# Optimization experiments

Hardware: AMD Instinct MI355X
Metric: run time of the kernel (lower is better)

The kernel has to match this reference:

```python
import jax, jax.numpy as jnp
import numpy as np
import math

N = 64
DIN = 2
DOUT = 2
D = 4
BATCH = 16384
EPS_DIV = 1e-6


def setup_inputs() -> dict:
    key = jax.random.key(0)
    k1, k2, k3 = jax.random.split(key, 3)
    x = jax.random.normal(k1, (BATCH, N, DIN), jnp.float32)
    # A scaled by 0.5 to keep 64-step products of DxD matrices inside float32 range
    A = jax.random.normal(k2, (N, D, D, DIN), jnp.float32) * 0.5
    B = jax.random.normal(k3, (N, D, D, DOUT, DIN), jnp.float32)
    scale = jnp.ones((1,), jnp.float32)
    return {"x": x, "A": A, "B": B, "scale": scale}


def _forward(x, A, B, scale):
    b, n, din = x.shape
    nbin = int(math.log(n - 1) / math.log(2.0)) + 1  # matches torch set_parallel_vars
    s = scale.reshape(())
    # per-site L2 normalization of input features (torch: X / ||X||, no eps)
    xn = x / jnp.linalg.norm(x, axis=-1, keepdims=True)
    M = jnp.einsum('bni,nlri->nblr', xn, A)  # [n, b, D, D] site matrices
    # binary tree of pairwise products: levels[l] has (n >> l) blocks covering 2^l sites
    levels = [M]
    cur = M
    for _ in range(nbin - 1):
        m = cur.shape[0]
        pair = cur.reshape(m // 2, 2, b, D, D)
        cur = jnp.einsum('pbij,pbjk->pbik', pair[:, 0], pair[:, 1])
        levels.append(cur)
    idx = jnp.arange(n)
    # Left prefix boundary vectors: vL[i] = e0^T * prod_{k<i} M_k (i=0 unused).
    # Built by walking the set bits of i (MSB->LSB), exactly like the torch
    # Bleft[nbin-1-j][xp[j]] indexing, but vectorized over all i at once.
    vL = jnp.zeros((n, b, D), M.dtype)
    startedL = jnp.zeros((n,), bool)
    for j in range(nbin):
        l = nbin - 1 - j                 # tree level for bit j
        bit = ((idx >> l) & 1).astype(bool)
        blk = 2 * (idx >> (l + 1))       # == xp[j] in torch
        Bl = levels[l][blk]              # [n, b, D, D]
        init = Bl[:, :, 0, :]            # left boundary row e0^T A
        step = jnp.einsum('nbi,nbij->nbj', vL, Bl)
        new = jnp.where(startedL[:, None, None], step, init)
        vL = jnp.where(bit[:, None, None], new, vL)
        startedL = startedL | bit
    vL = vL / (jnp.linalg.norm(vL, axis=-1, keepdims=True) + EPS_DIV)
    # Right suffix boundary vectors: vR[i] = (prod_{k=n-i}^{n-1} M_k) e0 (i=0 unused).
    # For n a power of two, Bright levels coincide with Bleft levels.
    vR = jnp.zeros((n, b, D), M.dtype)
    startedR = jnp.zeros((n,), bool)
    for j in range(nbin):
        l = nbin - 1 - j
        bit = ((idx >> l) & 1).astype(bool)
        nblk = n >> l
        blk = nblk - 1 - 2 * (idx >> (l + 1))  # index from the right end
        Bl = levels[l][blk]
        init = Bl[:, :, :, 0]            # right boundary column A e0
        step = jnp.einsum('nbij,nbj->nbi', Bl, vR)
        new = jnp.where(startedR[:, None, None], step, init)
        vR = jnp.where(bit[:, None, None], new, vR)
        startedR = startedR | bit
    vR = vR / (jnp.linalg.norm(vR, axis=-1, keepdims=True) + EPS_DIV)
    Aright = vR[::-1]  # Aright[i] = vR[n-1-i], valid for sites 0..n-2
    # Local operators H_i: boundary-contracted MPO tensors
    Hmid = jnp.einsum('nbi,niljk,nbl->nbjk', vL[1:n - 1], B[1:n - 1], Aright[1:n - 1])
    H0 = jnp.einsum('ljk,bl->bjk', B[0, 0], Aright[0])
    Hlast = jnp.einsum('bi,ijk->bjk', vL[n - 1], B[n - 1, :, 0])
    H = jnp.concatenate([H0[None], Hmid, Hlast[None]], axis=0)  # [n, b, dout, din]
    nrm = jnp.sqrt(jnp.sum(H * H, axis=(-2, -1), keepdims=True)) + EPS_DIV
    H = s * (H / nrm)
    H = jnp.where(jnp.isnan(H), 0.0, H)
    H = jax.nn.relu(H)                   # activation='relu'
    # apply local operator to normalized local input; out_norm='none'
    y = jnp.einsum('nbjk,bnk->bnj', H, xn)  # [b, n, dout]
    return y


def reference(x, A, B, scale):
    return _forward(x, A, B, scale)
```

## Files before the change

### kernel.cpp

```cpp
#include <hip/hip_runtime.h>
#include <math.h>


#define EPS 1e-6f

__global__ __launch_bounds__(256)
void tdvp_kernel(const float* __restrict__ x,
                 const float* __restrict__ A,
                 const float* __restrict__ Bw,
                 const float* __restrict__ scale,
                 float* __restrict__ y)
{
    __shared__ float sP[8 * 16 * 32];
    __shared__ float sXY[32 * 130];

    const int tid   = threadIdx.x;
    const int bb    = tid & 31;
    const int s     = tid >> 5;

    {
        const float4* xg = (const float4*)x + (size_t)blockIdx.x * 1024;
        #pragma unroll
        for (int it = 0; it < 4; ++it) {
            const int g = it * 256 + tid;
            const float4 v = xg[g];
            const int c = g >> 5, f = (g & 31) * 4;
            *(float2*)&sXY[c * 130 + f]     = make_float2(v.x, v.y);
            *(float2*)&sXY[c * 130 + f + 2] = make_float2(v.z, v.w);
        }
    }
    __syncthreads();

    const int n0 = s * 8;
    float xa[8], xc[8];
    #pragma unroll
    for (int k = 0; k < 8; ++k) {
        const float2 v = *(const float2*)&sXY[bb * 130 + s * 16 + 2 * k];
        const float inr = 1.f / sqrtf(v.x * v.x + v.y * v.y);
        xa[k] = v.x * inr; xc[k] = v.y * inr;
    }

    float M[8][16];
    #pragma unroll
    for (int k = 0; k < 8; ++k) {
        const float4* Aq = (const float4*)A + (size_t)(n0 + k) * 8;
        #pragma unroll
        for (int t = 0; t < 8; ++t) {
            const float4 q = Aq[t];
            M[k][2*t]     = fmaf(xc[k], q.y, xa[k] * q.x);
            M[k][2*t + 1] = fmaf(xc[k], q.w, xa[k] * q.z);
        }
    }

    {
        float P[16];
        #pragma unroll
        for (int e = 0; e < 16; ++e) P[e] = M[0][e];
        #pragma unroll
        for (int k = 1; k < 8; ++k) {
            float Pn[16];
            #pragma unroll
            for (int i = 0; i < 4; ++i) {
                #pragma unroll
                for (int j = 0; j < 4; ++j) {
                    float acc = P[i*4] * M[k][j];
                    acc = fmaf(P[i*4+1], M[k][4+j],  acc);
                    acc = fmaf(P[i*4+2], M[k][8+j],  acc);
                    acc = fmaf(P[i*4+3], M[k][12+j], acc);
                    Pn[i*4+j] = acc;
                }
            }
            #pragma unroll
            for (int e = 0; e < 16; ++e) P[e] = Pn[e];
        }
        float ss = 0.f;
        #pragma unroll
        for (int e = 0; e < 16; ++e) ss = fmaf(P[e], P[e], ss);
        const float rn = 1.f / (sqrtf(ss) + 1e-30f);
        #pragma unroll
        for (int e = 0; e < 16; ++e)
            sP[s * 512 + e * 32 + bb] = P[e] * rn;
    }
    __syncthreads();

    float v0 = 1.f, v1 = 0.f, v2 = 0.f, v3 = 0.f;
    #pragma unroll 1
    for (int t = 0; t < s; ++t) {
        const float* pp = &sP[t * 512 + bb];
        const float p0  = pp[0],      p1  = pp[32],     p2  = pp[64],     p3  = pp[96];
        const float p4  = pp[128],    p5  = pp[160],    p6  = pp[192],    p7  = pp[224];
        const float p8  = pp[256],    p9  = pp[288],    p10 = pp[320],    p11 = pp[352];
        const float p12 = pp[384],    p13 = pp[416],    p14 = pp[448],    p15 = pp[480];
        const float w0 = v0*p0 + v1*p4 + v2*p8  + v3*p12;
        const float w1 = v0*p1 + v1*p5 + v2*p9  + v3*p13;
        const float w2 = v0*p2 + v1*p6 + v2*p10 + v3*p14;
        const float w3 = v0*p3 + v1*p7 + v2*p11 + v3*p15;
        const float rn = 1.f / (sqrtf(w0*w0 + w1*w1 + w2*w2 + w3*w3) + 1e-30f);
        v0 = w0*rn; v1 = w1*rn; v2 = w2*rn; v3 = w3*rn;
    }
    float u0 = 1.f, u1 = 0.f, u2 = 0.f, u3 = 0.f;
    #pragma unroll 1
    for (int t = 7; t > s; --t) {
        const float* pp = &sP[t * 512 + bb];
        const float p0  = pp[0],      p1  = pp[32],     p2  = pp[64],     p3  = pp[96];
        const float p4  = pp[128],    p5  = pp[160],    p6  = pp[192],    p7  = pp[224];
        const float p8  = pp[256],    p9  = pp[288],    p10 = pp[320],    p11 = pp[352];
        const float p12 = pp[384],    p13 = pp[416],    p14 = pp[448],    p15 = pp[480];
        const float w0 = p0*u0  + p1*u1  + p2*u2  + p3*u3;
        const float w1 = p4*u0  + p5*u1  + p6*u2  + p7*u3;
        const float w2 = p8*u0  + p9*u1  + p10*u2 + p11*u3;
        const float w3 = p12*u0 + p13*u1 + p14*u2 + p15*u3;
        const float rn = 1.f / (sqrtf(w0*w0 + w1*w1 + w2*w2 + w3*w3) + 1e-30f);
        u0 = w0*rn; u1 = w1*rn; u2 = w2*rn; u3 = w3*rn;
    }

    float vlA[8], vlB[8], vlC[8], vlD[8];
    {
        float a0 = v0, a1 = v1, a2 = v2, a3 = v3;
        #pragma unroll
        for (int k = 0; k < 8; ++k) {
            vlA[k] = a0; vlB[k] = a1; vlC[k] = a2; vlD[k] = a3;
            if (k == 7) break;
            const float t0 = a0*M[k][0] + a1*M[k][4] + a2*M[k][8]  + a3*M[k][12];
            const float t1 = a0*M[k][1] + a1*M[k][5] + a2*M[k][9]  + a3*M[k][13];
            const float t2 = a0*M[k][2] + a1*M[k][6] + a2*M[k][10] + a3*M[k][14];
            const float t3 = a0*M[k][3] + a1*M[k][7] + a2*M[k][11] + a3*M[k][15];
            a0 = t0; a1 = t1; a2 = t2; a3 = t3;
        }
    }

    const float sc = scale[0];
    #pragma unroll
    for (int kk = 7; kk >= 0; --kk) {
        const int n = n0 + kk;

        const float arn = 1.f / (sqrtf(u0*u0 + u1*u1 + u2*u2 + u3*u3) + EPS);
        float aa0 = u0*arn, aa1 = u1*arn, aa2 = u2*arn, aa3 = u3*arn;
        if (n == 63) { aa0 = 1.f; aa1 = aa2 = aa3 = 0.f; }

        const float wn = 1.f / (sqrtf(vlA[kk]*vlA[kk] + vlB[kk]*vlB[kk] +
                                      vlC[kk]*vlC[kk] + vlD[kk]*vlD[kk]) + EPS);
        float vv0 = vlA[kk]*wn, vv1 = vlB[kk]*wn, vv2 = vlC[kk]*wn, vv3 = vlD[kk]*wn;
        if (n == 0) { vv0 = 1.f; vv1 = vv2 = vv3 = 0.f; }

        const float vv[4] = {vv0, vv1, vv2, vv3};
        const float aa[4] = {aa0, aa1, aa2, aa3};
        const float4* Bq = (const float4*)Bw + (size_t)n * 16;
        float H00 = 0.f, H01 = 0.f, H10 = 0.f, H11 = 0.f;
        #pragma unroll
        for (int half = 0; half < 2; ++half) {
            float4 bq[8];
            #pragma unroll
            for (int t = 0; t < 8; ++t) bq[t] = Bq[half * 8 + t];
            #pragma unroll
            for (int i2 = 0; i2 < 2; ++i2) {
                const int i = half * 2 + i2;
                #pragma unroll
                for (int l = 0; l < 4; ++l) {
                    const float  c = vv[i] * aa[l];
                    const float4 q = bq[i2 * 4 + l];
                    H00 = fmaf(c, q.x, H00);
                    H01 = fmaf(c, q.y, H01);
                    H10 = fmaf(c, q.z, H10);
                    H11 = fmaf(c, q.w, H11);
                }
            }
        }
        const float rh = sc / (sqrtf(H00*H00 + H01*H01 + H10*H10 + H11*H11) + EPS);
        H00 *= rh; H01 *= rh; H10 *= rh; H11 *= rh;
        if (__builtin_isnan(H00)) H00 = 0.f;
        if (__builtin_isnan(H01)) H01 = 0.f;
        if (__builtin_isnan(H10)) H10 = 0.f;
        if (__builtin_isnan(H11)) H11 = 0.f;
        H00 = fmaxf(H00, 0.f); H01 = fmaxf(H01, 0.f);
        H10 = fmaxf(H10, 0.f); H11 = fmaxf(H11, 0.f);

        float2 yo;
        yo.x = fmaf(H01, xc[kk], H00 * xa[kk]);
        yo.y = fmaf(H11, xc[kk], H10 * xa[kk]);
        *(float2*)&sXY[bb * 130 + 2 * n] = yo;

        if (kk > 0) {
            const float t0 = M[kk][0]*u0  + M[kk][1]*u1  + M[kk][2]*u2  + M[kk][3]*u3;
            const float t1 = M[kk][4]*u0  + M[kk][5]*u1  + M[kk][6]*u2  + M[kk][7]*u3;
            const float t2 = M[kk][8]*u0  + M[kk][9]*u1  + M[kk][10]*u2 + M[kk][11]*u3;
            const float t3 = M[kk][12]*u0 + M[kk][13]*u1 + M[kk][14]*u2 + M[kk][15]*u3;
            u0 = t0; u1 = t1; u2 = t2; u3 = t3;
        }
    }
    __syncthreads();

    {
        float4* yg = (float4*)y + (size_t)blockIdx.x * 1024;
        #pragma unroll
        for (int it = 0; it < 4; ++it) {
            const int g = it * 256 + tid;
            const int c = g >> 5, f = (g & 31) * 4;
            const float2 a = *(const float2*)&sXY[c * 130 + f];
            const float2 b = *(const float2*)&sXY[c * 130 + f + 2];
            yg[g] = make_float4(a.x, a.y, b.x, b.y);
        }
    }
}

extern "C" void kernel_launch(void* const* d_in, const int* in_sizes, int n_in,
                              void* d_out, int out_size, void* d_ws, size_t ws_size,
                              hipStream_t stream) {
    const float* x     = (const float*)d_in[0];
    const float* A     = (const float*)d_in[1];
    const float* B     = (const float*)d_in[2];
    const float* scale = (const float*)d_in[3];
    float* yp = (float*)d_out;
    const int batch  = in_sizes[0] / 128;
    const int blocks = batch / 32;
    tdvp_kernel<<<blocks, 256, 0, stream>>>(x, A, B, scale, yp);
}
```

Baseline: 82.35 us.

## Process two batch columns per thread with 128-thread blocks and recompute site matrices

```diff
diff --git a/kernel.cpp b/kernel.cpp
--- a/kernel.cpp
+++ b/kernel.cpp
@@ -4,149 +4,220 @@
 
 #define EPS 1e-6f
 
-__global__ __launch_bounds__(256)
+__global__ __launch_bounds__(128)
 void tdvp_kernel(const float* __restrict__ x,
                  const float* __restrict__ A,
                  const float* __restrict__ Bw,
                  const float* __restrict__ scale,
                  float* __restrict__ y)
 {
-    __shared__ float sP[8 * 16 * 32];
-    __shared__ float sXY[32 * 130];
-
-    const int tid   = threadIdx.x;
-    const int bb    = tid & 31;
-    const int s     = tid >> 5;
+    __shared__ float sBuf[32 * 130];
+
+    const int tid = threadIdx.x;
+    const int cp  = tid & 15;
+    const int s   = tid >> 4;
+    const int n0  = s * 8;
+    const int c0  = cp, c1 = cp + 16;
 
     {
         const float4* xg = (const float4*)x + (size_t)blockIdx.x * 1024;
         #pragma unroll
-        for (int it = 0; it < 4; ++it) {
-            const int g = it * 256 + tid;
+        for (int it = 0; it < 8; ++it) {
+            const int g = it * 128 + tid;
             const float4 v = xg[g];
             const int c = g >> 5, f = (g & 31) * 4;
-            *(float2*)&sXY[c * 130 + f]     = make_float2(v.x, v.y);
-            *(float2*)&sXY[c * 130 + f + 2] = make_float2(v.z, v.w);
-        }
-    }
-    __syncthreads();
-
-    const int n0 = s * 8;
-    float xa[8], xc[8];
+            *(float2*)&sBuf[c * 130 + f]     = make_float2(v.x, v.y);
+            *(float2*)&sBuf[c * 130 + f + 2] = make_float2(v.z, v.w);
+        }
+    }
+    __syncthreads();
+
+    float xa0[8], xc0[8], xa1[8], xc1[8];
     #pragma unroll
     for (int k = 0; k < 8; ++k) {
-        const float2 v = *(const float2*)&sXY[bb * 130 + s * 16 + 2 * k];
-        const float inr = 1.f / sqrtf(v.x * v.x + v.y * v.y);
-        xa[k] = v.x * inr; xc[k] = v.y * inr;
-    }
-
-    float M[8][16];
-    #pragma unroll
-    for (int k = 0; k < 8; ++k) {
-        const float4* Aq = (const float4*)A + (size_t)(n0 + k) * 8;
-        #pragma unroll
-        for (int t = 0; t < 8; ++t) {
-            const float4 q = Aq[t];
-            M[k][2*t]     = fmaf(xc[k], q.y, xa[k] * q.x);
-            M[k][2*t + 1] = fmaf(xc[k], q.w, xa[k] * q.z);
-        }
-    }
+        float2 v = *(const float2*)&sBuf[c0 * 130 + 2 * (n0 + k)];
+        float inr = 1.f / sqrtf(v.x * v.x + v.y * v.y);
+        xa0[k] = v.x * inr; xc0[k] = v.y * inr;
+        v = *(const float2*)&sBuf[c1 * 130 + 2 * (n0 + k)];
+        inr = 1.f / sqrtf(v.x * v.x + v.y * v.y);
+        xa1[k] = v.x * inr; xc1[k] = v.y * inr;
+    }
+    __syncthreads();
 
     {
-        float P[16];
-        #pragma unroll
-        for (int e = 0; e < 16; ++e) P[e] = M[0][e];
+        float P0[16], P1[16];
+        {
+            const float4* Aq = (const float4*)A + (size_t)n0 * 8;
+            #pragma unroll
+            for (int t = 0; t < 8; ++t) {
+                const float4 q = Aq[t];
+                P0[2*t]   = fmaf(xc0[0], q.y, xa0[0] * q.x);
+                P0[2*t+1] = fmaf(xc0[0], q.w, xa0[0] * q.z);
+                P1[2*t]   = fmaf(xc1[0], q.y, xa1[0] * q.x);
+                P1[2*t+1] = fmaf(xc1[0], q.w, xa1[0] * q.z);
+            }
+        }
         #pragma unroll
         for (int k = 1; k < 8; ++k) {
+            const float4* Ak = (const float4*)A + (size_t)(n0 + k) * 8;
+            float M0[16], M1[16];
+            #pragma unroll
+            for (int t = 0; t < 8; ++t) {
+                const float4 q = Ak[t];
+                M0[2*t]   = fmaf(xc0[k], q.y, xa0[k] * q.x);
+                M0[2*t+1] = fmaf(xc0[k], q.w, xa0[k] * q.z);
+                M1[2*t]   = fmaf(xc1[k], q.y, xa1[k] * q.x);
+                M1[2*t+1] = fmaf(xc1[k], q.w, xa1[k] * q.z);
+            }
             float Pn[16];
             #pragma unroll
-            for (int i = 0; i < 4; ++i) {
+            for (int i = 0; i < 4; ++i)
                 #pragma unroll
                 for (int j = 0; j < 4; ++j) {
-                    float acc = P[i*4] * M[k][j];
-                    acc = fmaf(P[i*4+1], M[k][4+j],  acc);
-                    acc = fmaf(P[i*4+2], M[k][8+j],  acc);
-                    acc = fmaf(P[i*4+3], M[k][12+j], acc);
+                    float acc = P0[i*4] * M0[j];
+                    acc = fmaf(P0[i*4+1], M0[4+j],  acc);
+                    acc = fmaf(P0[i*4+2], M0[8+j],  acc);
+                    acc = fmaf(P0[i*4+3], M0[12+j], acc);
                     Pn[i*4+j] = acc;
                 }
-            }
-            #pragma unroll
-            for (int e = 0; e < 16; ++e) P[e] = Pn[e];
-        }
-        float ss = 0.f;
-        #pragma unroll
-        for (int e = 0; e < 16; ++e) ss = fmaf(P[e], P[e], ss);
-        const float rn = 1.f / (sqrtf(ss) + 1e-30f);
-        #pragma unroll
-        for (int e = 0; e < 16; ++e)
-            sP[s * 512 + e * 32 + bb] = P[e] * rn;
-    }
-    __syncthreads();
-
-    float v0 = 1.f, v1 = 0.f, v2 = 0.f, v3 = 0.f;
+            #pragma unroll
+            for (int e = 0; e < 16; ++e) P0[e] = Pn[e];
+            #pragma unroll
+            for (int i = 0; i < 4; ++i)
+                #pragma unroll
+                for (int j = 0; j < 4; ++j) {
+                    float acc = P1[i*4] * M1[j];
+                    acc = fmaf(P1[i*4+1], M1[4+j],  acc);
+                    acc = fmaf(P1[i*4+2], M1[8+j],  acc);
+                    acc = fmaf(P1[i*4+3], M1[12+j], acc);
+                    Pn[i*4+j] = acc;
+                }
+            #pragma unroll
+            for (int e = 0; e < 16; ++e) P1[e] = Pn[e];
+        }
+        float s0 = 0.f, s1 = 0.f;
+        #pragma unroll
+        for (int e = 0; e < 16; ++e) { s0 = fmaf(P0[e], P0[e], s0);
+                                       s1 = fmaf(P1[e], P1[e], s1); }
+        const float r0 = 1.f / (sqrtf(s0) + 1e-30f);
+        const float r1 = 1.f / (sqrtf(s1) + 1e-30f);
+        #pragma unroll
+        for (int e = 0; e < 16; ++e) {
+            sBuf[s * 520 + e * 32 + c0] = P0[e] * r0;
+            sBuf[s * 520 + e * 32 + c1] = P1[e] * r1;
+        }
+    }
+    __syncthreads();
+
+    float v00 = 1.f, v01 = 0.f, v02 = 0.f, v03 = 0.f;
+    float v10 = 1.f, v11 = 0.f, v12 = 0.f, v13 = 0.f;
     #pragma unroll 1
     for (int t = 0; t < s; ++t) {
-        const float* pp = &sP[t * 512 + bb];
-        const float p0  = pp[0],      p1  = pp[32],     p2  = pp[64],     p3  = pp[96];
-        const float p4  = pp[128],    p5  = pp[160],    p6  = pp[192],    p7  = pp[224];
-        const float p8  = pp[256],    p9  = pp[288],    p10 = pp[320],    p11 = pp[352];
-        const float p12 = pp[384],    p13 = pp[416],    p14 = pp[448],    p15 = pp[480];
-        const float w0 = v0*p0 + v1*p4 + v2*p8  + v3*p12;
-        const float w1 = v0*p1 + v1*p5 + v2*p9  + v3*p13;
-        const float w2 = v0*p2 + v1*p6 + v2*p10 + v3*p14;
-        const float w3 = v0*p3 + v1*p7 + v2*p11 + v3*p15;
-        const float rn = 1.f / (sqrtf(w0*w0 + w1*w1 + w2*w2 + w3*w3) + 1e-30f);
-        v0 = w0*rn; v1 = w1*rn; v2 = w2*rn; v3 = w3*rn;
-    }
-    float u0 = 1.f, u1 = 0.f, u2 = 0.f, u3 = 0.f;
+        const float* pp = &sBuf[t * 520 + cp];
+        const float p0  = pp[0],    p1  = pp[32],   p2  = pp[64],   p3  = pp[96];
+        const float p4  = pp[128],  p5  = pp[160],  p6  = pp[192],  p7  = pp[224];
+        const float p8  = pp[256],  p9  = pp[288],  p10 = pp[320],  p11 = pp[352];
+        const float p12 = pp[384],  p13 = pp[416],  p14 = pp[448],  p15 = pp[480];
+        const float q0  = pp[16],   q1  = pp[48],   q2  = pp[80],   q3  = pp[112];
+        const float q4  = pp[144],  q5  = pp[176],  q6  = pp[208],  q7  = pp[240];
+        const float q8  = pp[272],  q9  = pp[304],  q10 = pp[336],  q11 = pp[368];
+        const float q12 = pp[400],  q13 = pp[432],  q14 = pp[464],  q15 = pp[496];
+        float w0 = v00*p0 + v01*p4 + v02*p8  + v03*p12;
+        float w1 = v00*p1 + v01*p5 + v02*p9  + v03*p13;
+        float w2 = v00*p2 + v01*p6 + v02*p10 + v03*p14;
+        float w3 = v00*p3 + v01*p7 + v02*p11 + v03*p15;
+        float rn = 1.f / (sqrtf(w0*w0 + w1*w1 + w2*w2 + w3*w3) + 1e-30f);
+        v00 = w0*rn; v01 = w1*rn; v02 = w2*rn; v03 = w3*rn;
+        w0 = v10*q0 + v11*q4 + v12*q8  + v13*q12;
+        w1 = v10*q1 + v11*q5 + v12*q9  + v13*q13;
+        w2 = v10*q2 + v11*q6 + v12*q10 + v13*q14;
+        w3 = v10*q3 + v11*q7 + v12*q11 + v13*q15;
+        rn = 1.f / (sqrtf(w0*w0 + w1*w1 + w2*w2 + w3*w3) + 1e-30f);
+        v10 = w0*rn; v11 = w1*rn; v12 = w2*rn; v13 = w3*rn;
+    }
+    float u00 = 1.f, u01 = 0.f, u02 = 0.f, u03 = 0.f;
+    float u10 = 1.f, u11 = 0.f, u12 = 0.f, u13 = 0.f;
     #pragma unroll 1
     for (int t = 7; t > s; --t) {
-        const float* pp = &sP[t * 512 + bb];
-        const float p0  = pp[0],      p1  = pp[32],     p2  = pp[64],     p3  = pp[96];
-        const float p4  = pp[128],    p5  = pp[160],    p6  = pp[192],    p7  = pp[224];
-        const float p8  = pp[256],    p9  = pp[288],    p10 = pp[320],    p11 = pp[352];
-        const float p12 = pp[384],    p13 = pp[416],    p14 = pp[448],    p15 = pp[480];
-        const float w0 = p0*u0  + p1*u1  + p2*u2  + p3*u3;
-        const float w1 = p4*u0  + p5*u1  + p6*u2  + p7*u3;
-        const float w2 = p8*u0  + p9*u1  + p10*u2 + p11*u3;
-        const float w3 = p12*u0 + p13*u1 + p14*u2 + p15*u3;
-        const float rn = 1.f / (sqrtf(w0*w0 + w1*w1 + w2*w2 + w3*w3) + 1e-30f);
-        u0 = w0*rn; u1 = w1*rn; u2 = w2*rn; u3 = w3*rn;
-    }
-
-    float vlA[8], vlB[8], vlC[8], vlD[8];
-    {
-        float a0 = v0, a1 = v1, a2 = v2, a3 = v3;
-        #pragma unroll
-        for (int k = 0; k < 8; ++k) {
-            vlA[k] = a0; vlB[k] = a1; vlC[k] = a2; vlD[k] = a3;
-            if (k == 7) break;
-            const float t0 = a0*M[k][0] + a1*M[k][4] + a2*M[k][8]  + a3*M[k][12];
-            const float t1 = a0*M[k][1] + a1*M[k][5] + a2*M[k][9]  + a3*M[k][13];
-            const float t2 = a0*M[k][2] + a1*M[k][6] + a2*M[k][10] + a3*M[k][14];
-            const float t3 = a0*M[k][3] + a1*M[k][7] + a2*M[k][11] + a3*M[k][15];
-            a0 = t0; a1 = t1; a2 = t2; a3 = t3;
-        }
-    }
-
-    const float sc = scale[0];
+        const float* pp = &sBuf[t * 520 + cp];
+        const float p0  = pp[0],    p1  = pp[32],   p2  = pp[64],   p3  = pp[96];
+        const float p4  = pp[128],  p5  = pp[160],  p6  = pp[192],  p7  = pp[224];
+        const float p8  = pp[256],  p9  = pp[288],  p10 = pp[320],  p11 = pp[352];
+        const float p12 = pp[384],  p13 = pp[416],  p14 = pp[448],  p15 = pp[480];
+        const float q0  = pp[16],   q1  = pp[48],   q2  = pp[80],   q3  = pp[112];
+        const float q4  = pp[144],  q5  = pp[176],  q6  = pp[208],  q7  = pp[240];
+        const float q8  = pp[272],  q9  = pp[304],  q10 = pp[336],  q11 = pp[368];
+        const float q12 = pp[400],  q13 = pp[432],  q14 = pp[464],  q15 = pp[496];
+        float w0 = p0*u00  + p1*u01  + p2*u02  + p3*u03;
+        float w1 = p4*u00  + p5*u01  + p6*u02  + p7*u03;
+        float w2 = p8*u00  + p9*u01  + p10*u02 + p11*u03;
+        float w3 = p12*u00 + p13*u01 + p14*u02 + p15*u03;
+        float rn = 1.f / (sqrtf(w0*w0 + w1*w1 + w2*w2 + w3*w3) + 1e-30f);
+        u00 = w0*rn; u01 = w1*rn; u02 = w2*rn; u03 = w3*rn;
+        w0 = q0*u10  + q1*u11  + q2*u12  + q3*u13;
+        w1 = q4*u10  + q5*u11  + q6*u12  + q7*u13;
+        w2 = q8*u10  + q9*u11  + q10*u12 + q11*u13;
+        w3 = q12*u10 + q13*u11 + q14*u12 + q15*u13;
+        rn = 1.f / (sqrtf(w0*w0 + w1*w1 + w2*w2 + w3*w3) + 1e-30f);
+        u10 = w0*rn; u11 = w1*rn; u12 = w2*rn; u13 = w3*rn;
+    }
+
+    float a0A[8], a0B[8], a0C[8], a0D[8];
+    float a1A[8], a1B[8], a1C[8], a1D[8];
     #pragma unroll
     for (int kk = 7; kk >= 0; --kk) {
         const int n = n0 + kk;
-
-        const float arn = 1.f / (sqrtf(u0*u0 + u1*u1 + u2*u2 + u3*u3) + EPS);
-        float aa0 = u0*arn, aa1 = u1*arn, aa2 = u2*arn, aa3 = u3*arn;
-        if (n == 63) { aa0 = 1.f; aa1 = aa2 = aa3 = 0.f; }
-
-        const float wn = 1.f / (sqrtf(vlA[kk]*vlA[kk] + vlB[kk]*vlB[kk] +
-                                      vlC[kk]*vlC[kk] + vlD[kk]*vlD[kk]) + EPS);
-        float vv0 = vlA[kk]*wn, vv1 = vlB[kk]*wn, vv2 = vlC[kk]*wn, vv3 = vlD[kk]*wn;
-        if (n == 0) { vv0 = 1.f; vv1 = vv2 = vv3 = 0.f; }
-
-        const float vv[4] = {vv0, vv1, vv2, vv3};
-        const float aa[4] = {aa0, aa1, aa2, aa3};
+        float rn = 1.f / (sqrtf(u00*u00 + u01*u01 + u02*u02 + u03*u03) + EPS);
+        a0A[kk] = u00*rn; a0B[kk] = u01*rn; a0C[kk] = u02*rn; a0D[kk] = u03*rn;
+        rn = 1.f / (sqrtf(u10*u10 + u11*u11 + u12*u12 + u13*u13) + EPS);
+        a1A[kk] = u10*rn; a1B[kk] = u11*rn; a1C[kk] = u12*rn; a1D[kk] = u13*rn;
+        if (n == 63) { a0A[kk] = 1.f; a0B[kk] = a0C[kk] = a0D[kk] = 0.f;
+                       a1A[kk] = 1.f; a1B[kk] = a1C[kk] = a1D[kk] = 0.f; }
+        if (kk > 0) {
+            const float4* Ak = (const float4*)A + (size_t)n * 8;
+            float M0[16], M1[16];
+            #pragma unroll
+            for (int t = 0; t < 8; ++t) {
+                const float4 q = Ak[t];
+                M0[2*t]   = fmaf(xc0[kk], q.y, xa0[kk] * q.x);
+                M0[2*t+1] = fmaf(xc0[kk], q.w, xa0[kk] * q.z);
+                M1[2*t]   = fmaf(xc1[kk], q.y, xa1[kk] * q.x);
+                M1[2*t+1] = fmaf(xc1[kk], q.w, xa1[kk] * q.z);
+            }
+            float t0 = M0[0]*u00  + M0[1]*u01  + M0[2]*u02  + M0[3]*u03;
+            float t1 = M0[4]*u00  + M0[5]*u01  + M0[6]*u02  + M0[7]*u03;
+            float t2 = M0[8]*u00  + M0[9]*u01  + M0[10]*u02 + M0[11]*u03;
+            float t3 = M0[12]*u00 + M0[13]*u01 + M0[14]*u02 + M0[15]*u03;
+            u00 = t0; u01 = t1; u02 = t2; u03 = t3;
+            t0 = M1[0]*u10  + M1[1]*u11  + M1[2]*u12  + M1[3]*u13;
+            t1 = M1[4]*u10  + M1[5]*u11  + M1[6]*u12  + M1[7]*u13;
+            t2 = M1[8]*u10  + M1[9]*u11  + M1[10]*u12 + M1[11]*u13;
+            t3 = M1[12]*u10 + M1[13]*u11 + M1[14]*u12 + M1[15]*u13;
+            u10 = t0; u11 = t1; u12 = t2; u13 = t3;
+        }
+    }
+    __syncthreads();
+
+    const float sc = scale[0];
+    #pragma unroll
+    for (int kk = 0; kk < 8; ++kk) {
+        const int n = n0 + kk;
+
+        float rn = 1.f / (sqrtf(v00*v00 + v01*v01 + v02*v02 + v03*v03) + EPS);
+        float vv0A = v00*rn, vv0B = v01*rn, vv0C = v02*rn, vv0D = v03*rn;
+        rn = 1.f / (sqrtf(v10*v10 + v11*v11 + v12*v12 + v13*v13) + EPS);
+        float vv1A = v10*rn, vv1B = v11*rn, vv1C = v12*rn, vv1D = v13*rn;
+        if (n == 0) { vv0A = 1.f; vv0B = vv0C = vv0D = 0.f;
+                      vv1A = 1.f; vv1B = vv1C = vv1D = 0.f; }
+
+        const float vv0[4] = {vv0A, vv0B, vv0C, vv0D};
+        const float vv1[4] = {vv1A, vv1B, vv1C, vv1D};
+        const float aa0[4] = {a0A[kk], a0B[kk], a0C[kk], a0D[kk]};
+        const float aa1[4] = {a1A[kk], a1B[kk], a1C[kk], a1D[kk]};
+
         const float4* Bq = (const float4*)Bw + (size_t)n * 16;
-        float H00 = 0.f, H01 = 0.f, H10 = 0.f, H11 = 0.f;
+        float G00 = 0.f, G01 = 0.f, G10 = 0.f, G11 = 0.f;
+        float K00 = 0.f, K01 = 0.f, K10 = 0.f, K11 = 0.f;
         #pragma unroll
         for (int half = 0; half < 2; ++half) {
             float4 bq[8];
@@ -157,35 +228,61 @@
                 const int i = half * 2 + i2;
                 #pragma unroll
                 for (int l = 0; l < 4; ++l) {
-                    const float  c = vv[i] * aa[l];
                     const float4 q = bq[i2 * 4 + l];
-                    H00 = fmaf(c, q.x, H00);
-                    H01 = fmaf(c, q.y, H01);
-                    H10 = fmaf(c, q.z, H10);
-                    H11 = fmaf(c, q.w, H11);
+                    const float ca = vv0[i] * aa0[l];
+                    G00 = fmaf(ca, q.x, G00); G01 = fmaf(ca, q.y, G01);
+                    G10 = fmaf(ca, q.z, G10); G11 = fmaf(ca, q.w, G11);
+                    const float cb = vv1[i] * aa1[l];
+                    K00 = fmaf(cb, q.x, K00); K01 = fmaf(cb, q.y, K01);
+                    K10 = fmaf(cb, q.z, K10); K11 = fmaf(cb, q.w, K11);
                 }
             }
         }
-        const float rh = sc / (sqrtf(H00*H00 + H01*H01 + H10*H10 + H11*H11) + EPS);
-        H00 *= rh; H01 *= rh; H10 *= rh; H11 *= rh;
-        if (__builtin_isnan(H00)) H00 = 0.f;
-        if (__builtin_isnan(H01)) H01 = 0.f;
-        if (__builtin_isnan(H10)) H10 = 0.f;
-        if (__builtin_isnan(H11)) H11 = 0.f;
-        H00 = fmaxf(H00, 0.f); H01 = fmaxf(H01, 0.f);
-        H10 = fmaxf(H10, 0.f); H11 = fmaxf(H11, 0.f);
-
-        float2 yo;
-        yo.x = fmaf(H01, xc[kk], H00 * xa[kk]);
-        yo.y = fmaf(H11, xc[kk], H10 * xa[kk]);
-        *(float2*)&sXY[bb * 130 + 2 * n] = yo;
-
-        if (kk > 0) {
-            const float t0 = M[kk][0]*u0  + M[kk][1]*u1  + M[kk][2]*u2  + M[kk][3]*u3;
-            const float t1 = M[kk][4]*u0  + M[kk][5]*u1  + M[kk][6]*u2  + M[kk][7]*u3;
-            const float t2 = M[kk][8]*u0  + M[kk][9]*u1  + M[kk][10]*u2 + M[kk][11]*u3;
-            const float t3 = M[kk][12]*u0 + M[kk][13]*u1 + M[kk][14]*u2 + M[kk][15]*u3;
-            u0 = t0; u1 = t1; u2 = t2; u3 = t3;
+        float rh = sc / (sqrtf(G00*G00 + G01*G01 + G10*G10 + G11*G11) + EPS);
+        G00 *= rh; G01 *= rh; G10 *= rh; G11 *= rh;
+        if (__builtin_isnan(G00)) G00 = 0.f;
+        if (__builtin_isnan(G01)) G01 = 0.f;
+        if (__builtin_isnan(G10)) G10 = 0.f;
+        if (__builtin_isnan(G11)) G11 = 0.f;
+        G00 = fmaxf(G00, 0.f); G01 = fmaxf(G01, 0.f);
+        G10 = fmaxf(G10, 0.f); G11 = fmaxf(G11, 0.f);
+        rh = sc / (sqrtf(K00*K00 + K01*K01 + K10*K10 + K11*K11) + EPS);
+        K00 *= rh; K01 *= rh; K10 *= rh; K11 *= rh;
+        if (__builtin_isnan(K00)) K00 = 0.f;
+        if (__builtin_isnan(K01)) K01 = 0.f;
+        if (__builtin_isnan(K10)) K10 = 0.f;
+        if (__builtin_isnan(K11)) K11 = 0.f;
+        K00 = fmaxf(K00, 0.f); K01 = fmaxf(K01, 0.f);
+        K10 = fmaxf(K10, 0.f); K11 = fmaxf(K11, 0.f);
+
+        *(float2*)&sBuf[c0 * 130 + 2 * n] =
+            make_float2(fmaf(G01, xc0[kk], G00 * xa0[kk]),
+                        fmaf(G11, xc0[kk], G10 * xa0[kk]));
+        *(float2*)&sBuf[c1 * 130 + 2 * n] =
+            make_float2(fmaf(K01, xc1[kk], K00 * xa1[kk]),
+                        fmaf(K11, xc1[kk], K10 * xa1[kk]));
+
+        if (kk < 7) {
+            const float4* Ak = (const float4*)A + (size_t)n * 8;
+            float M0[16], M1[16];
+            #pragma unroll
+            for (int t = 0; t < 8; ++t) {
+                const float4 q = Ak[t];
+                M0[2*t]   = fmaf(xc0[kk], q.y, xa0[kk] * q.x);
+                M0[2*t+1] = fmaf(xc0[kk], q.w, xa0[kk] * q.z);
+                M1[2*t]   = fmaf(xc1[kk], q.y, xa1[kk] * q.x);
+                M1[2*t+1] = fmaf(xc1[kk], q.w, xa1[kk] * q.z);
+            }
+            float t0 = v00*M0[0] + v01*M0[4] + v02*M0[8]  + v03*M0[12];
+            float t1 = v00*M0[1] + v01*M0[5] + v02*M0[9]  + v03*M0[13];
+            float t2 = v00*M0[2] + v01*M0[6] + v02*M0[10] + v03*M0[14];
+            float t3 = v00*M0[3] + v01*M0[7] + v02*M0[11] + v03*M0[15];
+            v00 = t0; v01 = t1; v02 = t2; v03 = t3;
+            t0 = v10*M1[0] + v11*M1[4] + v12*M1[8]  + v13*M1[12];
+            t1 = v10*M1[1] + v11*M1[5] + v12*M1[9]  + v13*M1[13];
+            t2 = v10*M1[2] + v11*M1[6] + v12*M1[10] + v13*M1[14];
+            t3 = v10*M1[3] + v11*M1[7] + v12*M1[11] + v13*M1[15];
+            v10 = t0; v11 = t1; v12 = t2; v13 = t3;
         }
     }
     __syncthreads();
@@ -193,11 +290,11 @@
     {
         float4* yg = (float4*)y + (size_t)blockIdx.x * 1024;
         #pragma unroll
-        for (int it = 0; it < 4; ++it) {
-            const int g = it * 256 + tid;
+        for (int it = 0; it < 8; ++it) {
+            const int g = it * 128 + tid;
             const int c = g >> 5, f = (g & 31) * 4;
-            const float2 a = *(const float2*)&sXY[c * 130 + f];
-            const float2 b = *(const float2*)&sXY[c * 130 + f + 2];
+            const float2 a = *(const float2*)&sBuf[c * 130 + f];
+            const float2 b = *(const float2*)&sBuf[c * 130 + f + 2];
             yg[g] = make_float4(a.x, a.y, b.x, b.y);
         }
     }
@@ -213,5 +310,5 @@
     float* yp = (float*)d_out;
     const int batch  = in_sizes[0] / 128;
     const int blocks = batch / 32;
-    tdvp_kernel<<<blocks, 256, 0, stream>>>(x, A, B, scale, yp);
+    tdvp_kernel<<<blocks, 128, 0, stream>>>(x, A, B, scale, yp);
 }
```

Result: slower. 123.7 us (+50.2%).

## Split chain into 16 segments of 4 sites, stage B in LDS

Applied to the files above, without the earlier changes.

```diff
diff --git a/kernel.cpp b/kernel.cpp
--- a/kernel.cpp
+++ b/kernel.cpp
@@ -4,45 +4,53 @@
 
 #define EPS 1e-6f
 
-__global__ __launch_bounds__(256)
+__global__ __launch_bounds__(256, 4)
 void tdvp_kernel(const float* __restrict__ x,
                  const float* __restrict__ A,
                  const float* __restrict__ Bw,
                  const float* __restrict__ scale,
                  float* __restrict__ y)
 {
-    __shared__ float sP[8 * 16 * 32];
-    __shared__ float sXY[32 * 130];
-
-    const int tid   = threadIdx.x;
-    const int bb    = tid & 31;
-    const int s     = tid >> 5;
-
-    {
-        const float4* xg = (const float4*)x + (size_t)blockIdx.x * 1024;
-        #pragma unroll
-        for (int it = 0; it < 4; ++it) {
+    __shared__ float sU[16 * 328];
+    __shared__ float sBf[64 * 68];
+
+    const int tid = threadIdx.x;
+    const int cb  = tid & 15;
+    const int s   = tid >> 4;
+    const int n0  = s * 4;
+
+    {
+        const float4* xg = (const float4*)x + (size_t)blockIdx.x * 512;
+        #pragma unroll
+        for (int it = 0; it < 2; ++it) {
             const int g = it * 256 + tid;
             const float4 v = xg[g];
             const int c = g >> 5, f = (g & 31) * 4;
-            *(float2*)&sXY[c * 130 + f]     = make_float2(v.x, v.y);
-            *(float2*)&sXY[c * 130 + f + 2] = make_float2(v.z, v.w);
-        }
-    }
-    __syncthreads();
-
-    const int n0 = s * 8;
-    float xa[8], xc[8];
-    #pragma unroll
-    for (int k = 0; k < 8; ++k) {
-        const float2 v = *(const float2*)&sXY[bb * 130 + s * 16 + 2 * k];
+            *(float2*)&sU[c * 130 + f]     = make_float2(v.x, v.y);
+            *(float2*)&sU[c * 130 + f + 2] = make_float2(v.z, v.w);
+        }
+        const float4* Bg = (const float4*)Bw;
+        #pragma unroll
+        for (int it = 0; it < 4; ++it) {
+            const int g = it * 256 + tid;
+            const int n = g >> 4, r = g & 15;
+            *(float4*)&sBf[n * 68 + r * 4] = Bg[g];
+        }
+    }
+    __syncthreads();
+
+    float xa[4], xc[4];
+    #pragma unroll
+    for (int k = 0; k < 4; ++k) {
+        const float2 v = *(const float2*)&sU[cb * 130 + 2 * (n0 + k)];
         const float inr = 1.f / sqrtf(v.x * v.x + v.y * v.y);
         xa[k] = v.x * inr; xc[k] = v.y * inr;
     }
-
-    float M[8][16];
-    #pragma unroll
-    for (int k = 0; k < 8; ++k) {
+    __syncthreads();
+
+    float M[4][16];
+    #pragma unroll
+    for (int k = 0; k < 4; ++k) {
         const float4* Aq = (const float4*)A + (size_t)(n0 + k) * 8;
         #pragma unroll
         for (int t = 0; t < 8; ++t) {
@@ -57,7 +65,7 @@
         #pragma unroll
         for (int e = 0; e < 16; ++e) P[e] = M[0][e];
         #pragma unroll
-        for (int k = 1; k < 8; ++k) {
+        for (int k = 1; k < 4; ++k) {
             float Pn[16];
             #pragma unroll
             for (int i = 0; i < 4; ++i) {
@@ -77,50 +85,52 @@
         #pragma unroll
         for (int e = 0; e < 16; ++e) ss = fmaf(P[e], P[e], ss);
         const float rn = 1.f / (sqrtf(ss) + 1e-30f);
-        #pragma unroll
-        for (int e = 0; e < 16; ++e)
-            sP[s * 512 + e * 32 + bb] = P[e] * rn;
+        float* pb = &sU[s * 328 + cb * 20];
+        *(float4*)(pb)      = make_float4(P[0]*rn,  P[1]*rn,  P[2]*rn,  P[3]*rn);
+        *(float4*)(pb + 4)  = make_float4(P[4]*rn,  P[5]*rn,  P[6]*rn,  P[7]*rn);
+        *(float4*)(pb + 8)  = make_float4(P[8]*rn,  P[9]*rn,  P[10]*rn, P[11]*rn);
+        *(float4*)(pb + 12) = make_float4(P[12]*rn, P[13]*rn, P[14]*rn, P[15]*rn);
     }
     __syncthreads();
 
     float v0 = 1.f, v1 = 0.f, v2 = 0.f, v3 = 0.f;
     #pragma unroll 1
     for (int t = 0; t < s; ++t) {
-        const float* pp = &sP[t * 512 + bb];
-        const float p0  = pp[0],      p1  = pp[32],     p2  = pp[64],     p3  = pp[96];
-        const float p4  = pp[128],    p5  = pp[160],    p6  = pp[192],    p7  = pp[224];
-        const float p8  = pp[256],    p9  = pp[288],    p10 = pp[320],    p11 = pp[352];
-        const float p12 = pp[384],    p13 = pp[416],    p14 = pp[448],    p15 = pp[480];
-        const float w0 = v0*p0 + v1*p4 + v2*p8  + v3*p12;
-        const float w1 = v0*p1 + v1*p5 + v2*p9  + v3*p13;
-        const float w2 = v0*p2 + v1*p6 + v2*p10 + v3*p14;
-        const float w3 = v0*p3 + v1*p7 + v2*p11 + v3*p15;
+        const float* pb = &sU[t * 328 + cb * 20];
+        const float4 r0 = *(const float4*)(pb);
+        const float4 r1 = *(const float4*)(pb + 4);
+        const float4 r2 = *(const float4*)(pb + 8);
+        const float4 r3 = *(const float4*)(pb + 12);
+        const float w0 = v0*r0.x + v1*r1.x + v2*r2.x + v3*r3.x;
+        const float w1 = v0*r0.y + v1*r1.y + v2*r2.y + v3*r3.y;
+        const float w2 = v0*r0.z + v1*r1.z + v2*r2.z + v3*r3.z;
+        const float w3 = v0*r0.w + v1*r1.w + v2*r2.w + v3*r3.w;
         const float rn = 1.f / (sqrtf(w0*w0 + w1*w1 + w2*w2 + w3*w3) + 1e-30f);
         v0 = w0*rn; v1 = w1*rn; v2 = w2*rn; v3 = w3*rn;
     }
     float u0 = 1.f, u1 = 0.f, u2 = 0.f, u3 = 0.f;
     #pragma unroll 1
-    for (int t = 7; t > s; --t) {
-        const float* pp = &sP[t * 512 + bb];
-        const float p0  = pp[0],      p1  = pp[32],     p2  = pp[64],     p3  = pp[96];
-        const float p4  = pp[128],    p5  = pp[160],    p6  = pp[192],    p7  = pp[224];
-        const float p8  = pp[256],    p9  = pp[288],    p10 = pp[320],    p11 = pp[352];
-        const float p12 = pp[384],    p13 = pp[416],    p14 = pp[448],    p15 = pp[480];
-        const float w0 = p0*u0  + p1*u1  + p2*u2  + p3*u3;
-        const float w1 = p4*u0  + p5*u1  + p6*u2  + p7*u3;
-        const float w2 = p8*u0  + p9*u1  + p10*u2 + p11*u3;
-        const float w3 = p12*u0 + p13*u1 + p14*u2 + p15*u3;
+    for (int t = 15; t > s; --t) {
+        const float* pb = &sU[t * 328 + cb * 20];
+        const float4 r0 = *(const float4*)(pb);
+        const float4 r1 = *(const float4*)(pb + 4);
+        const float4 r2 = *(const float4*)(pb + 8);
+        const float4 r3 = *(const float4*)(pb + 12);
+        const float w0 = r0.x*u0 + r0.y*u1 + r0.z*u2 + r0.w*u3;
+        const float w1 = r1.x*u0 + r1.y*u1 + r1.z*u2 + r1.w*u3;
+        const float w2 = r2.x*u0 + r2.y*u1 + r2.z*u2 + r2.w*u3;
+        const float w3 = r3.x*u0 + r3.y*u1 + r3.z*u2 + r3.w*u3;
         const float rn = 1.f / (sqrtf(w0*w0 + w1*w1 + w2*w2 + w3*w3) + 1e-30f);
         u0 = w0*rn; u1 = w1*rn; u2 = w2*rn; u3 = w3*rn;
     }
 
-    float vlA[8], vlB[8], vlC[8], vlD[8];
+    float vlA[4], vlB[4], vlC[4], vlD[4];
     {
         float a0 = v0, a1 = v1, a2 = v2, a3 = v3;
         #pragma unroll
-        for (int k = 0; k < 8; ++k) {
+        for (int k = 0; k < 4; ++k) {
             vlA[k] = a0; vlB[k] = a1; vlC[k] = a2; vlD[k] = a3;
-            if (k == 7) break;
+            if (k == 3) break;
             const float t0 = a0*M[k][0] + a1*M[k][4] + a2*M[k][8]  + a3*M[k][12];
             const float t1 = a0*M[k][1] + a1*M[k][5] + a2*M[k][9]  + a3*M[k][13];
             const float t2 = a0*M[k][2] + a1*M[k][6] + a2*M[k][10] + a3*M[k][14];
@@ -130,8 +140,9 @@
     }
 
     const float sc = scale[0];
-    #pragma unroll
-    for (int kk = 7; kk >= 0; --kk) {
+    float yo[8];
+    #pragma unroll
+    for (int kk = 3; kk >= 0; --kk) {
         const int n = n0 + kk;
 
         const float arn = 1.f / (sqrtf(u0*u0 + u1*u1 + u2*u2 + u3*u3) + EPS);
@@ -145,25 +156,21 @@
 
         const float vv[4] = {vv0, vv1, vv2, vv3};
         const float aa[4] = {aa0, aa1, aa2, aa3};
-        const float4* Bq = (const float4*)Bw + (size_t)n * 16;
+        const float* Bq = &sBf[n * 68];
         float H00 = 0.f, H01 = 0.f, H10 = 0.f, H11 = 0.f;
         #pragma unroll
-        for (int half = 0; half < 2; ++half) {
-            float4 bq[8];
-            #pragma unroll
-            for (int t = 0; t < 8; ++t) bq[t] = Bq[half * 8 + t];
-            #pragma unroll
-            for (int i2 = 0; i2 < 2; ++i2) {
-                const int i = half * 2 + i2;
-                #pragma unroll
-                for (int l = 0; l < 4; ++l) {
-                    const float  c = vv[i] * aa[l];
-                    const float4 q = bq[i2 * 4 + l];
-                    H00 = fmaf(c, q.x, H00);
-                    H01 = fmaf(c, q.y, H01);
-                    H10 = fmaf(c, q.z, H10);
-                    H11 = fmaf(c, q.w, H11);
-                }
+        for (int i = 0; i < 4; ++i) {
+            float4 bq[4];
+            #pragma unroll
+            for (int l = 0; l < 4; ++l) bq[l] = *(const float4*)(Bq + (i*4 + l)*4);
+            #pragma unroll
+            for (int l = 0; l < 4; ++l) {
+                const float  c = vv[i] * aa[l];
+                const float4 q = bq[l];
+                H00 = fmaf(c, q.x, H00);
+                H01 = fmaf(c, q.y, H01);
+                H10 = fmaf(c, q.z, H10);
+                H11 = fmaf(c, q.w, H11);
             }
         }
         const float rh = sc / (sqrtf(H00*H00 + H01*H01 + H10*H10 + H11*H11) + EPS);
@@ -175,10 +182,8 @@
         H00 = fmaxf(H00, 0.f); H01 = fmaxf(H01, 0.f);
         H10 = fmaxf(H10, 0.f); H11 = fmaxf(H11, 0.f);
 
-        float2 yo;
-        yo.x = fmaf(H01, xc[kk], H00 * xa[kk]);
-        yo.y = fmaf(H11, xc[kk], H10 * xa[kk]);
-        *(float2*)&sXY[bb * 130 + 2 * n] = yo;
+        yo[2*kk]     = fmaf(H01, xc[kk], H00 * xa[kk]);
+        yo[2*kk + 1] = fmaf(H11, xc[kk], H10 * xa[kk]);
 
         if (kk > 0) {
             const float t0 = M[kk][0]*u0  + M[kk][1]*u1  + M[kk][2]*u2  + M[kk][3]*u3;
@@ -190,14 +195,19 @@
     }
     __syncthreads();
 
-    {
-        float4* yg = (float4*)y + (size_t)blockIdx.x * 1024;
-        #pragma unroll
-        for (int it = 0; it < 4; ++it) {
+    #pragma unroll
+    for (int kk = 0; kk < 4; ++kk)
+        *(float2*)&sU[cb * 130 + 2 * (n0 + kk)] =
+            make_float2(yo[2*kk], yo[2*kk + 1]);
+    __syncthreads();
+    {
+        float4* yg = (float4*)y + (size_t)blockIdx.x * 512;
+        #pragma unroll
+        for (int it = 0; it < 2; ++it) {
             const int g = it * 256 + tid;
             const int c = g >> 5, f = (g & 31) * 4;
-            const float2 a = *(const float2*)&sXY[c * 130 + f];
-            const float2 b = *(const float2*)&sXY[c * 130 + f + 2];
+            const float2 a = *(const float2*)&sU[c * 130 + f];
+            const float2 b = *(const float2*)&sU[c * 130 + f + 2];
             yg[g] = make_float4(a.x, a.y, b.x, b.y);
         }
     }
@@ -212,6 +222,6 @@
     const float* scale = (const float*)d_in[3];
     float* yp = (float*)d_out;
     const int batch  = in_sizes[0] / 128;
-    const int blocks = batch / 32;
+    const int blocks = batch / 16;
     tdvp_kernel<<<blocks, 256, 0, stream>>>(x, A, B, scale, yp);
 }
```

Result: slower. 84.31 us (+2.4%).
